# Performance work log

Measured on AMD Instinct MI355X. Metric: run time of the kernel, lower is better.

The kernel has to match this reference:

```python
import jax, jax.numpy as jnp
import numpy as np

EMBED = 1024
HEADS = 16
HEAD_DIM = EMBED // HEADS
SCALE = HEAD_DIM ** -0.5


def setup_inputs() -> dict:
    key = jax.random.key(0)
    ks = jax.random.split(key, 11)
    B, S, D = 2, 2048, EMBED
    s = D ** -0.5
    return {
        "Q": jax.random.normal(ks[0], (B, S, D), jnp.float32),
        "K": jax.random.normal(ks[1], (B, S, D), jnp.float32),
        "V": jax.random.normal(ks[2], (B, S, D), jnp.float32),
        "Wq": jax.random.normal(ks[3], (D, D), jnp.float32) * s,
        "bq": jax.random.normal(ks[4], (D,), jnp.float32) * 0.01,
        "Wk": jax.random.normal(ks[5], (D, D), jnp.float32) * s,
        "bk": jax.random.normal(ks[6], (D,), jnp.float32) * 0.01,
        "Wv": jax.random.normal(ks[7], (D, D), jnp.float32) * s,
        "bv": jax.random.normal(ks[8], (D,), jnp.float32) * 0.01,
        "Wo": jax.random.normal(ks[9], (D, D), jnp.float32) * s,
        "bo": jax.random.normal(ks[10], (D,), jnp.float32) * 0.01,
    }


def reference(Q, K, V, Wq, bq, Wk, bk, Wv, bv, Wo, bo):
    N, S, D = Q.shape
    H, Hd = HEADS, HEAD_DIM
    # linear projections (x @ W + b), then split heads: [N, S, H, Hd]
    q = (Q @ Wq + bq).reshape(N, S, H, Hd)
    k = (K @ Wk + bk).reshape(N, S, H, Hd)
    v = (V @ Wv + bv).reshape(N, S, H, Hd)
    # scaled dot-product attention, full [N,H,S,S] scores as in the original
    energy = jnp.einsum('nqhd,nkhd->nhqk', q, k) * SCALE
    attn = jax.nn.softmax(energy, axis=3)
    out = jnp.einsum('nhql,nlhd->nqhd', attn, v).reshape(N, S, D)
    return out @ Wo + bo
```

## Files before the change

kernel.cpp:

```cpp
#include <hip/hip_runtime.h>
#include <cstdint>


typedef _Float16 h8 __attribute__((ext_vector_type(8)));
typedef float f4 __attribute__((ext_vector_type(4)));
typedef float f16v __attribute__((ext_vector_type(16)));
typedef unsigned int u32x4 __attribute__((ext_vector_type(4)));
typedef const unsigned int __attribute__((address_space(1)))* gp1_t;
typedef unsigned int __attribute__((address_space(3)))* lp3_t;

#define FSWZ(r) ((((r) ^ ((r) >> 3))) & 7)

__device__ __forceinline__ void gld_lds16(const void* g, const void* l) {
  __builtin_amdgcn_global_load_lds((gp1_t)(uintptr_t)g,
                                   (lp3_t)(unsigned int)(uintptr_t)l, 16, 0, 0);
}
__device__ __forceinline__ unsigned pkh(float a, float b) {
  return __builtin_bit_cast(unsigned, __builtin_amdgcn_cvt_pkrtz(a, b));
}
__device__ __forceinline__ void plswap(unsigned& a, unsigned& b) {
  asm volatile("v_permlane32_swap_b32 %0, %1" : "+v"(a), "+v"(b));
}


__global__ void cvt_x3(const float* __restrict__ a, const float* __restrict__ b,
                       const float* __restrict__ c, _Float16* __restrict__ out) {
  const int z = blockIdx.z;
  const float* in = (z == 0) ? a : (z == 1) ? b : c;
  _Float16* o = out + (size_t)z * 4194304;
  const int i = (blockIdx.x * 256 + threadIdx.x) * 8;
  float4 u = *(const float4*)(in + i);
  float4 w = *(const float4*)(in + i + 4);
  h8 r = {(_Float16)u.x, (_Float16)u.y, (_Float16)u.z, (_Float16)u.w,
          (_Float16)w.x, (_Float16)w.y, (_Float16)w.z, (_Float16)w.w};
  *(h8*)(o + i) = r;
}

__global__ void cvt_w4(const float* __restrict__ wq, const float* __restrict__ wk,
                       const float* __restrict__ wv, const float* __restrict__ wo,
                       _Float16* __restrict__ WT) {
  const int z = blockIdx.z;
  const float* W = (z == 0) ? wq : (z == 1) ? wk : (z == 2) ? wv : wo;
  _Float16* o = WT + (size_t)z * 1048576;
  const int k = blockIdx.x * 256 + threadIdx.x;
  const int n0 = blockIdx.y * 4;
  float4 w = *(const float4*)(W + (size_t)k * 1024 + n0);
  o[(size_t)(n0 + 0) * 1024 + k] = (_Float16)w.x;
  o[(size_t)(n0 + 1) * 1024 + k] = (_Float16)w.y;
  o[(size_t)(n0 + 2) * 1024 + k] = (_Float16)w.z;
  o[(size_t)(n0 + 3) * 1024 + k] = (_Float16)w.w;
}


#define G_STAGE(BUF, KT)                                                       \
  do {                                                                         \
    _Pragma("unroll") for (int rr_ = 0; rr_ < 4; ++rr_) {                      \
      const int idx_ = rr_ * 256 + tid;                                        \
      const int r_ = idx_ >> 3, g_ = idx_ & 7;                                 \
      const int lb_ = (rr_ * 256 + wave * 64) * 8;                             \
      gld_lds16(A16 + (size_t)(row0 + r_) * 1024 + (KT) * 64 + (g_ ^ FSWZ(r_)) * 8,\
                &As[BUF][lb_]);                                                \
      gld_lds16(Bt + (size_t)(col0 + r_) * 1024 + (KT) * 64 + (g_ ^ FSWZ(r_)) * 8,\
                &Bs[BUF][lb_]);                                                \
    }                                                                          \
  } while (0)

__global__ __launch_bounds__(256, 2) void gemm_qkv(const _Float16* __restrict__ X16,
                                                   const _Float16* __restrict__ WT,
                                                   const float* __restrict__ bq,
                                                   const float* __restrict__ bk,
                                                   const float* __restrict__ bv,
                                                   _Float16* __restrict__ qkv16) {
  __shared__ _Float16 As[2][8192];
  __shared__ _Float16 Bs[2][8192];
  const int z = blockIdx.z;
  const _Float16* A16 = X16 + (size_t)z * 4194304;
  const _Float16* Bt = WT + (size_t)z * 1048576;
  const float* bias = (z == 0) ? bq : (z == 1) ? bk : bv;
  _Float16* out16 = qkv16 + (size_t)z * 4194304;
  const float scl = (z == 0) ? 0.18033688f : 1.0f;
  const int tid = threadIdx.x;
  const int wave = tid >> 6, lane = tid & 63;
  const int lg = lane >> 4, ll = lane & 15;
  const int wr = wave >> 1, wc = wave & 1;
  const int row0 = blockIdx.x * 128, col0 = blockIdx.y * 128;
  f4 acc[4][4] = {};
  G_STAGE(0, 0);
  __syncthreads();
  int cur = 0;
  for (int kt = 0; kt < 16; ++kt) {
    if (kt + 1 < 16) G_STAGE(cur ^ 1, kt + 1);
#pragma unroll
    for (int kk = 0; kk < 2; ++kk) {
      h8 af[4], bf[4];
#pragma unroll
      for (int mi = 0; mi < 4; ++mi) {
        const int r = wr * 64 + mi * 16 + ll;
        af[mi] = *(const h8*)&As[cur][r * 64 + (((kk * 4 + lg) ^ FSWZ(r)) << 3)];
      }
#pragma unroll
      for (int ni = 0; ni < 4; ++ni) {
        const int r = wc * 64 + ni * 16 + ll;
        bf[ni] = *(const h8*)&Bs[cur][r * 64 + (((kk * 4 + lg) ^ FSWZ(r)) << 3)];
      }
#pragma unroll
      for (int mi = 0; mi < 4; ++mi)
#pragma unroll
        for (int ni = 0; ni < 4; ++ni)
          acc[mi][ni] = __builtin_amdgcn_mfma_f32_16x16x32_f16(af[mi], bf[ni],
                                                               acc[mi][ni], 0, 0, 0);
    }
    __syncthreads();
    cur ^= 1;
  }
#pragma unroll
  for (int ni = 0; ni < 4; ++ni) {
    const int c = col0 + wc * 64 + ni * 16 + ll;
    const float bv = bias[c];
#pragma unroll
    for (int mi = 0; mi < 4; ++mi) {
#pragma unroll
      for (int i = 0; i < 4; ++i) {
        const int r = row0 + wr * 64 + mi * 16 + lg * 4 + i;
        const float val = (acc[mi][ni][i] + bv) * scl;
        const int b = r >> 11, s = r & 2047, h = c >> 6, hd = c & 63;
        out16[((size_t)((b * 16 + h) * 2048 + s)) * 64 + hd] = (_Float16)val;
      }
    }
  }
}


#define GO_STAGE(BUF, KT)                                                      \
  do {                                                                         \
    _Pragma("unroll") for (int rr_ = 0; rr_ < 4; ++rr_) {                      \
      const int idx_ = rr_ * 256 + tid;                                        \
      const int r_ = idx_ >> 3, g_ = idx_ & 7;                                 \
      gld_lds16(A16 + (size_t)(row0 + r_) * 1024 + (KT) * 64 + (g_ ^ FSWZ(r_)) * 8,\
                &As[BUF][(rr_ * 256 + wave * 64) * 8]);                        \
    }                                                                          \
    _Pragma("unroll") for (int rr_ = 0; rr_ < 2; ++rr_) {                      \
      const int idx_ = rr_ * 256 + tid;                                        \
      const int r_ = idx_ >> 3, g_ = idx_ & 7;                                 \
      gld_lds16(WoT + (size_t)(col0 + r_) * 1024 + (KT) * 64 + (g_ ^ FSWZ(r_)) * 8,\
                &Bs[BUF][(rr_ * 256 + wave * 64) * 8]);                        \
    }                                                                          \
  } while (0)

__global__ __launch_bounds__(256, 3) void gemm_out_k(const _Float16* __restrict__ A16,
                                                     const _Float16* __restrict__ WoT,
                                                     const float* __restrict__ bo,
                                                     float* __restrict__ out) {
  __shared__ _Float16 As[2][8192];
  __shared__ _Float16 Bs[2][4096];
  const int tid = threadIdx.x;
  const int wave = tid >> 6, lane = tid & 63;
  const int lg = lane >> 4, ll = lane & 15;
  const int wr = wave >> 1, wc = wave & 1;
  const int row0 = blockIdx.x * 128, col0 = blockIdx.y * 64;
  f4 acc[4][2] = {};
  GO_STAGE(0, 0);
  __syncthreads();
  int cur = 0;
  for (int kt = 0; kt < 16; ++kt) {
    if (kt + 1 < 16) GO_STAGE(cur ^ 1, kt + 1);
#pragma unroll
    for (int kk = 0; kk < 2; ++kk) {
      h8 af[4], bf[2];
#pragma unroll
      for (int mi = 0; mi < 4; ++mi) {
        const int r = wr * 64 + mi * 16 + ll;
        af[mi] = *(const h8*)&As[cur][r * 64 + (((kk * 4 + lg) ^ FSWZ(r)) << 3)];
      }
#pragma unroll
      for (int ni = 0; ni < 2; ++ni) {
        const int r = wc * 32 + ni * 16 + ll;
        bf[ni] = *(const h8*)&Bs[cur][r * 64 + (((kk * 4 + lg) ^ FSWZ(r)) << 3)];
      }
#pragma unroll
      for (int mi = 0; mi < 4; ++mi)
#pragma unroll
        for (int ni = 0; ni < 2; ++ni)
          acc[mi][ni] = __builtin_amdgcn_mfma_f32_16x16x32_f16(af[mi], bf[ni],
                                                               acc[mi][ni], 0, 0, 0);
    }
    __syncthreads();
    cur ^= 1;
  }
#pragma unroll
  for (int ni = 0; ni < 2; ++ni) {
    const int c = col0 + wc * 32 + ni * 16 + ll;
    const float bv = bo[c];
#pragma unroll
    for (int mi = 0; mi < 4; ++mi)
#pragma unroll
      for (int i = 0; i < 4; ++i) {
        const int r = row0 + wr * 64 + mi * 16 + lg * 4 + i;
        out[(size_t)r * 1024 + c] = acc[mi][ni][i] + bv;
      }
  }
}


#define STAGE_K(BUF, KT)                                                      \
  do {                                                                        \
    _Pragma("unroll") for (int rr_ = 0; rr_ < 2; ++rr_) {                     \
      const int idx_ = rr_ * 256 + tid;                                       \
      const int r_ = idx_ >> 3, g_ = idx_ & 7;                                \
      gld_lds16(kbp + (size_t)((KT) * 64 + r_) * 64 + ((g_ ^ FSWZ(r_)) * 8),  \
                &Ks[BUF][(rr_ * 256 + wave * 64) * 8]);                       \
    }                                                                         \
  } while (0)

#define LOAD_V(KT)                                                            \
  do {                                                                        \
    const _Float16* vp_ = vbp + (size_t)((KT) * 64 + vkey0) * 64 + vhd0;      \
    va = *(const uint4*)vp_;                                                  \
    vc = *(const uint4*)(vp_ + 64);                                           \
  } while (0)

#define WRITE_V(BUF)                                                          \
  do {                                                                        \
    const unsigned short* pa_ = (const unsigned short*)&va;                   \
    const unsigned short* pc_ = (const unsigned short*)&vc;                   \
    _Pragma("unroll") for (int j_ = 0; j_ < 8; ++j_) {                        \
      const int row_ = vhd0 + j_;                                             \
      *(unsigned*)&Vt[BUF][row_ * 64 + (((vkey0 >> 3) ^ FSWZ(row_)) << 3) +   \
                           (vkey0 & 7)] =                                     \
          (unsigned)pa_[j_] | ((unsigned)pc_[j_] << 16);                      \
    }                                                                         \
  } while (0)

#define QK_COMPUTE(BUF, S0, S1)                                               \
  do {                                                                        \
    S0 = (f16v){};                                                            \
    S1 = (f16v){};                                                            \
    _Pragma("unroll") for (int kc_ = 0; kc_ < 4; ++kc_) {                     \
      const int c_ = kc_ * 2 + hi;                                            \
      h8 k0_ = *(const h8*)&Ks[BUF][l31 * 64 + ((c_ ^ FSWZ(l31)) << 3)];      \
      h8 k1_ = *(const h8*)&Ks[BUF][(32 + l31) * 64 +                         \
                                    ((c_ ^ FSWZ(32 + l31)) << 3)];            \
      h8 qf_ = (kc_ == 0) ? qf0 : (kc_ == 1) ? qf1 : (kc_ == 2) ? qf2 : qf3;  \
      S0 = __builtin_amdgcn_mfma_f32_32x32x16_f16(k0_, qf_, S0, 0, 0, 0);     \
      S1 = __builtin_amdgcn_mfma_f32_32x32x16_f16(k1_, qf_, S1, 0, 0, 0);     \
    }                                                                         \
  } while (0)

#define PACK_AF(DST, SX, PP)                                                  \
  do {                                                                        \
    unsigned wA = pkh(SX[(PP) + 0], SX[(PP) + 1]);                            \
    unsigned wB = pkh(SX[(PP) + 2], SX[(PP) + 3]);                            \
    unsigned wC = pkh(SX[(PP) + 4], SX[(PP) + 5]);                            \
    unsigned wD = pkh(SX[(PP) + 6], SX[(PP) + 7]);                            \
    plswap(wA, wC);                                                           \
    plswap(wB, wD);                                                           \
    DST = (u32x4){wA, wB, wC, wD};                                            \
  } while (0)

#define SM_PK(S0, S1)                                                         \
  do {                                                                        \
    float t_[8];                                                              \
    _Pragma("unroll") for (int j2_ = 0; j2_ < 8; ++j2_)                       \
        t_[j2_] = fmaxf(fmaxf(S0[j2_], S0[j2_ + 8]),                          \
                        fmaxf(S1[j2_], S1[j2_ + 8]));                         \
    float pm_ = fmaxf(fmaxf(fmaxf(t_[0], t_[1]), fmaxf(t_[2], t_[3])),        \
                      fmaxf(fmaxf(t_[4], t_[5]), fmaxf(t_[6], t_[7])));       \
    pm_ = fmaxf(pm_, __shfl_xor(pm_, 32));                                    \
    if (__any(pm_ > mval + 8.0f)) {                                           \
      const float mn_ = fmaxf(mval, pm_);                                     \
      const float f_ = __builtin_amdgcn_exp2f(mval - mn_);                    \
      mval = mn_;                                                             \
      lsum *= f_;                                                             \
      Fb[wave][l31] = f_;                                                     \
      const f4 fr0_ = *(const f4*)&Fb[wave][0 + 4 * hi];                      \
      const f4 fr1_ = *(const f4*)&Fb[wave][8 + 4 * hi];                      \
      const f4 fr2_ = *(const f4*)&Fb[wave][16 + 4 * hi];                     \
      const f4 fr3_ = *(const f4*)&Fb[wave][24 + 4 * hi];                     \
      _Pragma("unroll") for (int r_ = 0; r_ < 16; ++r_) {                     \
        const float fx_ =                                                     \
            (r_ < 4 ? fr0_ : r_ < 8 ? fr1_ : r_ < 12 ? fr2_ : fr3_)[r_ & 3];  \
        acc0[r_] *= fx_;                                                      \
        acc1[r_] *= fx_;                                                      \
      }                                                                       \
    }                                                                         \
    _Pragma("unroll") for (int r_ = 0; r_ < 16; ++r_) {                       \
      S0[r_] = __builtin_amdgcn_exp2f(S0[r_] - mval);                         \
      S1[r_] = __builtin_amdgcn_exp2f(S1[r_] - mval);                         \
    }                                                                         \
    float z_[8];                                                              \
    _Pragma("unroll") for (int j2_ = 0; j2_ < 8; ++j2_)                       \
        z_[j2_] = (S0[j2_] + S0[j2_ + 8]) + (S1[j2_] + S1[j2_ + 8]);          \
    lsum += ((z_[0] + z_[1]) + (z_[2] + z_[3])) +                             \
            ((z_[4] + z_[5]) + (z_[6] + z_[7]));                              \
    PACK_AF(afr[0], S0, 0);                                                   \
    PACK_AF(afr[1], S0, 8);                                                   \
    PACK_AF(afr[2], S1, 0);                                                   \
    PACK_AF(afr[3], S1, 8);                                                   \
  } while (0)

#define PV_APPLY(BUF)                                                         \
  do {                                                                        \
    _Pragma("unroll") for (int i_ = 0; i_ < 4; ++i_) {                        \
      const int c_ = i_ * 2 + hi;                                             \
      h8 vf0_ = *(const h8*)&Vt[BUF][l31 * 64 + ((c_ ^ FSWZ(l31)) << 3)];     \
      h8 vf1_ = *(const h8*)&Vt[BUF][(32 + l31) * 64 +                        \
                                     ((c_ ^ FSWZ(32 + l31)) << 3)];           \
      h8 af_ = __builtin_bit_cast(h8, afr[i_]);                               \
      acc0 = __builtin_amdgcn_mfma_f32_32x32x16_f16(af_, vf0_, acc0, 0, 0, 0);\
      acc1 = __builtin_amdgcn_mfma_f32_32x32x16_f16(af_, vf1_, acc1, 0, 0, 0);\
    }                                                                         \
  } while (0)

__global__ __launch_bounds__(256, 2) void attn_kernel(
    const _Float16* __restrict__ q16, const _Float16* __restrict__ k16,
    const _Float16* __restrict__ v16, _Float16* __restrict__ aout) {
  __shared__ _Float16 Ks[2][4096];
  __shared__ _Float16 Vt[2][4096];
  __shared__ float Fb[4][32];
  const int tid = threadIdx.x;
  const int wave = tid >> 6, lane = tid & 63;
  const int l31 = lane & 31, hi = lane >> 5;
  const int blk = blockIdx.x;
  const int xcd = blk & 7, j = blk >> 3;
  const int bh = xcd * 4 + (j >> 4);
  const int qb = j & 15;
  const int q0w = qb * 128 + wave * 32;
  const _Float16* qbp = q16 + (size_t)bh * 131072;
  const _Float16* kbp = k16 + (size_t)bh * 131072;
  const _Float16* vbp = v16 + (size_t)bh * 131072;
  const int vkey0 = (tid & 31) * 2, vhd0 = (tid >> 5) * 8;

  h8 qf0 = *(const h8*)(qbp + (size_t)(q0w + l31) * 64 + 0 + hi * 8);
  h8 qf1 = *(const h8*)(qbp + (size_t)(q0w + l31) * 64 + 16 + hi * 8);
  h8 qf2 = *(const h8*)(qbp + (size_t)(q0w + l31) * 64 + 32 + hi * 8);
  h8 qf3 = *(const h8*)(qbp + (size_t)(q0w + l31) * 64 + 48 + hi * 8);

  f16v acc0 = {}, acc1 = {};
  f16v sr0 = {}, sr1 = {};
  u32x4 afr[4];
  float mval = -1e30f, lsum = 0.f;
  uint4 va, vc;

  STAGE_K(0, 0);
  LOAD_V(0);
  WRITE_V(0);
  __syncthreads();
  QK_COMPUTE(0, sr0, sr1);
  STAGE_K(1, 1);
  LOAD_V(1);
  WRITE_V(1);
  SM_PK(sr0, sr1);
  __syncthreads();

  for (int t = 0; t < 31; ++t) {
    const int A = t & 1, B = A ^ 1;
    if (t + 2 < 32) LOAD_V(t + 2);
    __builtin_amdgcn_s_setprio(1);
    QK_COMPUTE(B, sr0, sr1);
    PV_APPLY(A);
    __builtin_amdgcn_s_setprio(0);
    __builtin_amdgcn_sched_barrier(0);
    __syncthreads();
    if (t + 2 < 32) { STAGE_K(A, t + 2); WRITE_V(A); }
    SM_PK(sr0, sr1);
    __syncthreads();
  }
  PV_APPLY(1);

  lsum += __shfl_xor(lsum, 32);
  const float inv = 1.0f / lsum;
  Fb[wave][l31] = inv;
  const f4 ir0 = *(const f4*)&Fb[wave][0 + 4 * hi];
  const f4 ir1 = *(const f4*)&Fb[wave][8 + 4 * hi];
  const f4 ir2 = *(const f4*)&Fb[wave][16 + 4 * hi];
  const f4 ir3 = *(const f4*)&Fb[wave][24 + 4 * hi];
  const int b = bh >> 4, h = bh & 15;
#pragma unroll
  for (int r = 0; r < 16; ++r) {
    const float fx = (r < 4 ? ir0 : r < 8 ? ir1 : r < 12 ? ir2 : ir3)[r & 3];
    const int srow = q0w + (r & 3) + 8 * (r >> 2) + 4 * hi;
    _Float16* op = aout + ((size_t)(b * 2048 + srow)) * 1024 + h * 64 + l31;
    op[0] = (_Float16)(acc0[r] * fx);
    op[32] = (_Float16)(acc1[r] * fx);
  }
}


extern "C" void kernel_launch(void* const* d_in, const int* in_sizes, int n_in,
                              void* d_out, int out_size, void* d_ws, size_t ws_size,
                              hipStream_t stream) {
  const float* Q  = (const float*)d_in[0];
  const float* K  = (const float*)d_in[1];
  const float* V  = (const float*)d_in[2];
  const float* Wq = (const float*)d_in[3];
  const float* bq = (const float*)d_in[4];
  const float* Wk = (const float*)d_in[5];
  const float* bk = (const float*)d_in[6];
  const float* Wv = (const float*)d_in[7];
  const float* bv = (const float*)d_in[8];
  const float* Wo = (const float*)d_in[9];
  const float* bo = (const float*)d_in[10];

  _Float16* H      = (_Float16*)d_ws;
  _Float16* X16    = H;
  _Float16* WT     = H + 12582912;
  _Float16* qkv16  = H + 16777216;
  _Float16* aout16 = H + 29360128;
  float* out = (float*)d_out;

  cvt_x3<<<dim3(2048, 1, 3), 256, 0, stream>>>(Q, K, V, X16);
  cvt_w4<<<dim3(4, 256, 4), 256, 0, stream>>>(Wq, Wk, Wv, Wo, WT);
  gemm_qkv<<<dim3(32, 8, 3), 256, 0, stream>>>(X16, WT, bq, bk, bv, qkv16);
  attn_kernel<<<dim3(512), 256, 0, stream>>>(qkv16, qkv16 + 4194304,
                                             qkv16 + 8388608, aout16);
  gemm_out_k<<<dim3(32, 16), 256, 0, stream>>>(aout16, WT + 3145728, bo, out);
}
```

Measured before the change: 129.5 us.

## Load K/V attention fragments directly from global memory, pre-transposing V in projection

The V projection kernel now writes V in a transposed [b,h,hd,s] layout. The attention kernel drops its LDS staging and barriers for K and V and instead loads MFMA fragments straight from global memory into registers, double-buffering K fragments across tiles. This removes the LDS writes, the in-register V transpose and most syncthreads, at the cost of more global/L2 traffic since each wave reloads K/V independently, higher register pressure, and less latency hiding between load and use.

```diff
diff --git a/kernel.cpp b/kernel.cpp
--- a/kernel.cpp
+++ b/kernel.cpp
@@ -124,7 +124,11 @@
         const int r = row0 + wr * 64 + mi * 16 + lg * 4 + i;
         const float val = (acc[mi][ni][i] + bv) * scl;
         const int b = r >> 11, s = r & 2047, h = c >> 6, hd = c & 63;
-        out16[((size_t)((b * 16 + h) * 2048 + s)) * 64 + hd] = (_Float16)val;
+        if (z == 2) {
+          out16[((size_t)((b * 16 + h) * 64 + hd)) * 2048 + s] = (_Float16)val;
+        } else {
+          out16[((size_t)((b * 16 + h) * 2048 + s)) * 64 + hd] = (_Float16)val;
+        }
       }
     }
   }
@@ -202,47 +206,35 @@
 }
 
 
-#define STAGE_K(BUF, KT)                                                      \
-  do {                                                                        \
-    _Pragma("unroll") for (int rr_ = 0; rr_ < 2; ++rr_) {                     \
-      const int idx_ = rr_ * 256 + tid;                                       \
-      const int r_ = idx_ >> 3, g_ = idx_ & 7;                                \
-      gld_lds16(kbp + (size_t)((KT) * 64 + r_) * 64 + ((g_ ^ FSWZ(r_)) * 8),  \
-                &Ks[BUF][(rr_ * 256 + wave * 64) * 8]);                       \
-    }                                                                         \
-  } while (0)
-
-#define LOAD_V(KT)                                                            \
-  do {                                                                        \
-    const _Float16* vp_ = vbp + (size_t)((KT) * 64 + vkey0) * 64 + vhd0;      \
-    va = *(const uint4*)vp_;                                                  \
-    vc = *(const uint4*)(vp_ + 64);                                           \
-  } while (0)
-
-#define WRITE_V(BUF)                                                          \
-  do {                                                                        \
-    const unsigned short* pa_ = (const unsigned short*)&va;                   \
-    const unsigned short* pc_ = (const unsigned short*)&vc;                   \
-    _Pragma("unroll") for (int j_ = 0; j_ < 8; ++j_) {                        \
-      const int row_ = vhd0 + j_;                                             \
-      *(unsigned*)&Vt[BUF][row_ * 64 + (((vkey0 >> 3) ^ FSWZ(row_)) << 3) +   \
-                           (vkey0 & 7)] =                                     \
-          (unsigned)pa_[j_] | ((unsigned)pc_[j_] << 16);                      \
-    }                                                                         \
-  } while (0)
-
-#define QK_COMPUTE(BUF, S0, S1)                                               \
+#define K_FRAGS(DST, KT)                                                      \
+  do {                                                                        \
+    _Pragma("unroll") for (int i_ = 0; i_ < 4; ++i_) {                        \
+      const _Float16* kp_ =                                                   \
+          kbp + (size_t)((KT) * 64 + l31) * 64 + (i_ * 2 + hi) * 8;           \
+      DST[2 * i_] = *(const h8*)kp_;                                          \
+      DST[2 * i_ + 1] = *(const h8*)(kp_ + 2048);                \
+    }                                                                         \
+  } while (0)
+
+#define V_FRAGS(DST, KT)                                                      \
+  do {                                                                        \
+    _Pragma("unroll") for (int i_ = 0; i_ < 4; ++i_) {                        \
+      const _Float16* vp_ =                                                   \
+          vtp + (size_t)l31 * 2048 + (KT) * 64 + (i_ * 2 + hi) * 8;           \
+      DST[2 * i_] = *(const h8*)vp_;                                          \
+      DST[2 * i_ + 1] = *(const h8*)(vp_ + 65536);                \
+    }                                                                         \
+  } while (0)
+
+#define QK_C(KF, S0, S1)                                                      \
   do {                                                                        \
     S0 = (f16v){};                                                            \
     S1 = (f16v){};                                                            \
     _Pragma("unroll") for (int kc_ = 0; kc_ < 4; ++kc_) {                     \
-      const int c_ = kc_ * 2 + hi;                                            \
-      h8 k0_ = *(const h8*)&Ks[BUF][l31 * 64 + ((c_ ^ FSWZ(l31)) << 3)];      \
-      h8 k1_ = *(const h8*)&Ks[BUF][(32 + l31) * 64 +                         \
-                                    ((c_ ^ FSWZ(32 + l31)) << 3)];            \
       h8 qf_ = (kc_ == 0) ? qf0 : (kc_ == 1) ? qf1 : (kc_ == 2) ? qf2 : qf3;  \
-      S0 = __builtin_amdgcn_mfma_f32_32x32x16_f16(k0_, qf_, S0, 0, 0, 0);     \
-      S1 = __builtin_amdgcn_mfma_f32_32x32x16_f16(k1_, qf_, S1, 0, 0, 0);     \
+      S0 = __builtin_amdgcn_mfma_f32_32x32x16_f16(KF[2 * kc_], qf_, S0, 0, 0, 0);\
+      S1 = __builtin_amdgcn_mfma_f32_32x32x16_f16(KF[2 * kc_ + 1], qf_, S1,   \
+                                                  0, 0, 0);                   \
     }                                                                         \
   } while (0)
 
@@ -298,24 +290,33 @@
     PACK_AF(afr[3], S1, 8);                                                   \
   } while (0)
 
-#define PV_APPLY(BUF)                                                         \
+#define PV_C(VF)                                                              \
   do {                                                                        \
     _Pragma("unroll") for (int i_ = 0; i_ < 4; ++i_) {                        \
-      const int c_ = i_ * 2 + hi;                                             \
-      h8 vf0_ = *(const h8*)&Vt[BUF][l31 * 64 + ((c_ ^ FSWZ(l31)) << 3)];     \
-      h8 vf1_ = *(const h8*)&Vt[BUF][(32 + l31) * 64 +                        \
-                                     ((c_ ^ FSWZ(32 + l31)) << 3)];           \
       h8 af_ = __builtin_bit_cast(h8, afr[i_]);                               \
-      acc0 = __builtin_amdgcn_mfma_f32_32x32x16_f16(af_, vf0_, acc0, 0, 0, 0);\
-      acc1 = __builtin_amdgcn_mfma_f32_32x32x16_f16(af_, vf1_, acc1, 0, 0, 0);\
-    }                                                                         \
+      acc0 = __builtin_amdgcn_mfma_f32_32x32x16_f16(af_, VF[2 * i_], acc0,    \
+                                                    0, 0, 0);                 \
+      acc1 = __builtin_amdgcn_mfma_f32_32x32x16_f16(af_, VF[2 * i_ + 1],      \
+                                                    acc1, 0, 0, 0);           \
+    }                                                                         \
+  } while (0)
+
+#define TILE_STEP(KC, KN, T)                                                  \
+  do {                                                                        \
+    if ((T) + 1 < 32) K_FRAGS(KN, (T) + 1);                                   \
+    V_FRAGS(vf, (T));                                                         \
+    __builtin_amdgcn_s_setprio(1);                                            \
+    QK_C(KC, sr0, sr1);                                                       \
+    __builtin_amdgcn_s_setprio(0);                                            \
+    SM_PK(sr0, sr1);                                                          \
+    __builtin_amdgcn_s_setprio(1);                                            \
+    PV_C(vf);                                                                 \
+    __builtin_amdgcn_s_setprio(0);                                            \
   } while (0)
 
 __global__ __launch_bounds__(256, 2) void attn_kernel(
     const _Float16* __restrict__ q16, const _Float16* __restrict__ k16,
-    const _Float16* __restrict__ v16, _Float16* __restrict__ aout) {
-  __shared__ _Float16 Ks[2][4096];
-  __shared__ _Float16 Vt[2][4096];
+    const _Float16* __restrict__ v16t, _Float16* __restrict__ aout) {
   __shared__ float Fb[4][32];
   const int tid = threadIdx.x;
   const int wave = tid >> 6, lane = tid & 63;
@@ -327,8 +328,7 @@
   const int q0w = qb * 128 + wave * 32;
   const _Float16* qbp = q16 + (size_t)bh * 131072;
   const _Float16* kbp = k16 + (size_t)bh * 131072;
-  const _Float16* vbp = v16 + (size_t)bh * 131072;
-  const int vkey0 = (tid & 31) * 2, vhd0 = (tid >> 5) * 8;
+  const _Float16* vtp = v16t + (size_t)bh * 131072;
 
   h8 qf0 = *(const h8*)(qbp + (size_t)(q0w + l31) * 64 + 0 + hi * 8);
   h8 qf1 = *(const h8*)(qbp + (size_t)(q0w + l31) * 64 + 16 + hi * 8);
@@ -336,36 +336,17 @@
   h8 qf3 = *(const h8*)(qbp + (size_t)(q0w + l31) * 64 + 48 + hi * 8);
 
   f16v acc0 = {}, acc1 = {};
-  f16v sr0 = {}, sr1 = {};
+  f16v sr0, sr1;
   u32x4 afr[4];
+  h8 kA[8], kB[8], vf[8];
   float mval = -1e30f, lsum = 0.f;
-  uint4 va, vc;
-
-  STAGE_K(0, 0);
-  LOAD_V(0);
-  WRITE_V(0);
-  __syncthreads();
-  QK_COMPUTE(0, sr0, sr1);
-  STAGE_K(1, 1);
-  LOAD_V(1);
-  WRITE_V(1);
-  SM_PK(sr0, sr1);
-  __syncthreads();
-
-  for (int t = 0; t < 31; ++t) {
-    const int A = t & 1, B = A ^ 1;
-    if (t + 2 < 32) LOAD_V(t + 2);
-    __builtin_amdgcn_s_setprio(1);
-    QK_COMPUTE(B, sr0, sr1);
-    PV_APPLY(A);
-    __builtin_amdgcn_s_setprio(0);
-    __builtin_amdgcn_sched_barrier(0);
-    __syncthreads();
-    if (t + 2 < 32) { STAGE_K(A, t + 2); WRITE_V(A); }
-    SM_PK(sr0, sr1);
-    __syncthreads();
-  }
-  PV_APPLY(1);
+
+  K_FRAGS(kA, 0);
+  for (int th = 0; th < 16; ++th) {
+    TILE_STEP(kA, kB, th * 2);
+    TILE_STEP(kB, kA, th * 2 + 1);
+    if ((th & 3) == 3 && th != 15) __syncthreads();
+  }
 
   lsum += __shfl_xor(lsum, 32);
   const float inv = 1.0f / lsum;
```

After: 197.6 us. 1.53x slower.

## Store V transposed in projection and triple-buffer K/V with async LDS loads

Applied to the files above, without the earlier changes.

The V projection epilogue now writes V head-major with the head dimension outer and the sequence inner, so the attention kernel can stage V^T tiles straight into LDS with global_load_lds instead of loading to registers and transposing by hand. K and V now use a three-stage LDS ring, which drops one barrier per iteration and issues loads two tiles ahead. The cost is more LDS, which may limit two blocks per CU, and strided scattered fp16 stores in the projection epilogue. Correctness of a single barrier with three buffers depends on when the async loads complete.

```diff
diff --git a/kernel.cpp b/kernel.cpp
--- a/kernel.cpp
+++ b/kernel.cpp
@@ -124,7 +124,11 @@
         const int r = row0 + wr * 64 + mi * 16 + lg * 4 + i;
         const float val = (acc[mi][ni][i] + bv) * scl;
         const int b = r >> 11, s = r & 2047, h = c >> 6, hd = c & 63;
-        out16[((size_t)((b * 16 + h) * 2048 + s)) * 64 + hd] = (_Float16)val;
+        if (z == 2) {
+          out16[((size_t)((b * 16 + h) * 64 + hd)) * 2048 + s] = (_Float16)val;
+        } else {
+          out16[((size_t)((b * 16 + h) * 2048 + s)) * 64 + hd] = (_Float16)val;
+        }
       }
     }
   }
@@ -212,22 +216,13 @@
     }                                                                         \
   } while (0)
 
-#define LOAD_V(KT)                                                            \
-  do {                                                                        \
-    const _Float16* vp_ = vbp + (size_t)((KT) * 64 + vkey0) * 64 + vhd0;      \
-    va = *(const uint4*)vp_;                                                  \
-    vc = *(const uint4*)(vp_ + 64);                                           \
-  } while (0)
-
-#define WRITE_V(BUF)                                                          \
-  do {                                                                        \
-    const unsigned short* pa_ = (const unsigned short*)&va;                   \
-    const unsigned short* pc_ = (const unsigned short*)&vc;                   \
-    _Pragma("unroll") for (int j_ = 0; j_ < 8; ++j_) {                        \
-      const int row_ = vhd0 + j_;                                             \
-      *(unsigned*)&Vt[BUF][row_ * 64 + (((vkey0 >> 3) ^ FSWZ(row_)) << 3) +   \
-                           (vkey0 & 7)] =                                     \
-          (unsigned)pa_[j_] | ((unsigned)pc_[j_] << 16);                      \
+#define STAGE_V(BUF, KT)                                                      \
+  do {                                                                        \
+    _Pragma("unroll") for (int rr_ = 0; rr_ < 2; ++rr_) {                     \
+      const int idx_ = rr_ * 256 + tid;                                       \
+      const int r_ = idx_ >> 3, g_ = idx_ & 7;                                \
+      gld_lds16(vtp + (size_t)r_ * 2048 + (KT) * 64 + ((g_ ^ FSWZ(r_)) * 8),  \
+                &Vt[BUF][(rr_ * 256 + wave * 64) * 8]);                       \
     }                                                                         \
   } while (0)
 
@@ -313,9 +308,9 @@
 
 __global__ __launch_bounds__(256, 2) void attn_kernel(
     const _Float16* __restrict__ q16, const _Float16* __restrict__ k16,
-    const _Float16* __restrict__ v16, _Float16* __restrict__ aout) {
-  __shared__ _Float16 Ks[2][4096];
-  __shared__ _Float16 Vt[2][4096];
+    const _Float16* __restrict__ v16t, _Float16* __restrict__ aout) {
+  __shared__ _Float16 Ks[3][4096];
+  __shared__ _Float16 Vt[3][4096];
   __shared__ float Fb[4][32];
   const int tid = threadIdx.x;
   const int wave = tid >> 6, lane = tid & 63;
@@ -327,8 +322,7 @@
   const int q0w = qb * 128 + wave * 32;
   const _Float16* qbp = q16 + (size_t)bh * 131072;
   const _Float16* kbp = k16 + (size_t)bh * 131072;
-  const _Float16* vbp = v16 + (size_t)bh * 131072;
-  const int vkey0 = (tid & 31) * 2, vhd0 = (tid >> 5) * 8;
+  const _Float16* vtp = v16t + (size_t)bh * 131072;
 
   h8 qf0 = *(const h8*)(qbp + (size_t)(q0w + l31) * 64 + 0 + hi * 8);
   h8 qf1 = *(const h8*)(qbp + (size_t)(q0w + l31) * 64 + 16 + hi * 8);
@@ -336,36 +330,30 @@
   h8 qf3 = *(const h8*)(qbp + (size_t)(q0w + l31) * 64 + 48 + hi * 8);
 
   f16v acc0 = {}, acc1 = {};
-  f16v sr0 = {}, sr1 = {};
+  f16v sr0, sr1;
   u32x4 afr[4];
   float mval = -1e30f, lsum = 0.f;
-  uint4 va, vc;
 
   STAGE_K(0, 0);
-  LOAD_V(0);
-  WRITE_V(0);
+  STAGE_V(0, 0);
+  STAGE_K(1, 1);
+  STAGE_V(1, 1);
   __syncthreads();
   QK_COMPUTE(0, sr0, sr1);
-  STAGE_K(1, 1);
-  LOAD_V(1);
-  WRITE_V(1);
   SM_PK(sr0, sr1);
-  __syncthreads();
-
+
+  int s0 = 0, s1 = 1, s2 = 2;
   for (int t = 0; t < 31; ++t) {
-    const int A = t & 1, B = A ^ 1;
-    if (t + 2 < 32) LOAD_V(t + 2);
+    if (t < 30) { STAGE_K(s2, t + 2); STAGE_V(s2, t + 2); }
     __builtin_amdgcn_s_setprio(1);
-    QK_COMPUTE(B, sr0, sr1);
-    PV_APPLY(A);
+    QK_COMPUTE(s1, sr0, sr1);
+    PV_APPLY(s0);
     __builtin_amdgcn_s_setprio(0);
-    __builtin_amdgcn_sched_barrier(0);
-    __syncthreads();
-    if (t + 2 < 32) { STAGE_K(A, t + 2); WRITE_V(A); }
     SM_PK(sr0, sr1);
     __syncthreads();
-  }
-  PV_APPLY(1);
+    const int tmp = s0; s0 = s1; s1 = s2; s2 = tmp;
+  }
+  PV_APPLY(s0);
 
   lsum += __shfl_xor(lsum, 32);
   const float inv = 1.0f / lsum;
```

New measurement: 133.9 us. 1.03x slower.
